# Kernel tuning notes

Hardware: AMD Instinct MI355X
Metric: run time of the kernel (lower is better)

The kernel has to match this reference:

```python
import jax, jax.numpy as jnp
import numpy as np

S, X, G = 2048, 2048, 2
INPUT_SIZE = (3, 32, 32)
F = int(np.prod(INPUT_SIZE))


def setup_inputs() -> dict:
    key = jax.random.key(0)
    k1, k2, k3 = jax.random.split(key, 3)
    samples = jax.random.normal(k1, (S,) + INPUT_SIZE, dtype=jnp.float32)
    x = jax.random.normal(k2, (X,) + INPUT_SIZE, dtype=jnp.float32)
    # per-feature std per gradation, kept in [0.1, 1.0) like ranges_std scaling
    std = jax.random.uniform(k3, (G, F), dtype=jnp.float32, minval=0.1, maxval=1.0)
    return {"samples": samples, "x": x, "std": std}


def reference(samples, x, std):
    # samples: [S, C, H, W], x: [X, C, H, W], std: [G, F]
    G_, F_ = std.shape
    s = samples.reshape(samples.shape[0], F_)  # [S, F]
    xf = x.reshape(x.shape[0], F_)             # [X, F]
    w = 1.0 / (std * std)                       # [G, F] precision
    # per-gradation normalizer: -0.5*F*log(2pi) - sum_f log(std)
    const = -0.5 * F_ * jnp.log(2.0 * jnp.pi) - jnp.sum(jnp.log(std), axis=1)  # [G]
    # sum_f -0.5*((s-x)/std)^2 expanded: -0.5*(s^2 w - 2 s w x + x^2 w)
    A = jnp.einsum('sf,gf->gs', s * s, w)        # [G, S]
    C = jnp.einsum('xf,gf->gx', xf * xf, w)      # [G, X]
    B = jnp.einsum('sf,gf,xf->gsx', s, w, xf)    # [G, S, X] cross term
    logits = -0.5 * (A[:, :, None] - 2.0 * B + C[:, None, :]) + const[:, None, None]
    lp = jax.nn.logsumexp(logits, axis=2)        # over x (mixture components)
    lp = jax.nn.logsumexp(lp, axis=0)            # over gradations
    return lp - jnp.log(jnp.float32(x.shape[0] * G_))
```

## Files before the change

### kernel.cpp

```cpp
#include <hip/hip_runtime.h>
#include <math.h>

#define S_N 2048
#define X_N 2048
#define G_N 2
#define F_N 3072

#define TM 128
#define TN 128
#define BK 64
#define ITERS (F_N / BK)

typedef __bf16 bf16;
typedef __bf16 bf16x4 __attribute__((ext_vector_type(4)));
typedef __bf16 bf16x8 __attribute__((ext_vector_type(8)));
typedef float f32x4 __attribute__((ext_vector_type(4)));
typedef int i32x4 __attribute__((ext_vector_type(4)));

#define LGKM_BARRIER() asm volatile("s_waitcnt lgkmcnt(0)\n\ts_barrier" ::: "memory")

__global__ void k_const(const float* __restrict__ stdv, float* __restrict__ constg,
                        float* __restrict__ rinv) {
  int g = blockIdx.x;
  int t = threadIdx.x;
  float s = 0.f;
  for (int f = t; f < F_N; f += 256) {
    float v = stdv[g * F_N + f];
    rinv[g * F_N + f] = 1.0f / v;
    s += logf(v);
  }
  for (int o = 32; o; o >>= 1) s += __shfl_xor(s, o);
  __shared__ float red[4];
  int w = t >> 6, l = t & 63;
  if (l == 0) red[w] = s;
  __syncthreads();
  if (t == 0) {
    float tot = red[0] + red[1] + red[2] + red[3];
    constg[g] = -0.5f * (float)F_N * 1.8378770664093453f - tot;
  }
}

__global__ void k_prep(const float* __restrict__ samples, const float* __restrict__ xin,
                       const float* __restrict__ rinv,
                       bf16* __restrict__ U, bf16* __restrict__ V,
                       float* __restrict__ A, float* __restrict__ C) {
  int r = blockIdx.x;
  int t = threadIdx.x;
  bool isS = (r < S_N);
  const float* src = isS ? (samples + (size_t)r * F_N) : (xin + (size_t)(r - S_N) * F_N);
  float4 row[3];
#pragma unroll
  for (int j = 0; j < 3; ++j) row[j] = ((const float4*)src)[t + j * 256];

  __shared__ float red[4];
  int w = t >> 6, l = t & 63;

  for (int g = 0; g < G_N; ++g) {
    const float4* sd = (const float4*)(rinv + (size_t)g * F_N);
    bf16* dst = isS ? (U + ((size_t)g * S_N + r) * F_N)
                    : (V + ((size_t)g * X_N + (r - S_N)) * F_N);
    float acc = 0.f;
#pragma unroll
    for (int j = 0; j < 3; ++j) {
      float4 d = sd[t + j * 256];
      float u0 = row[j].x * d.x;
      float u1 = row[j].y * d.y;
      float u2 = row[j].z * d.z;
      float u3 = row[j].w * d.w;
      bf16x4 b;
      b[0] = (bf16)u0; b[1] = (bf16)u1; b[2] = (bf16)u2; b[3] = (bf16)u3;
      float f0 = (float)b[0], f1 = (float)b[1], f2 = (float)b[2], f3 = (float)b[3];
      acc += f0 * f0 + f1 * f1 + f2 * f2 + f3 * f3;
      ((bf16x4*)dst)[t + j * 256] = b;
    }
    for (int o = 32; o; o >>= 1) acc += __shfl_xor(acc, o);
    __syncthreads();
    if (l == 0) red[w] = acc;
    __syncthreads();
    if (t == 0) {
      float tot = red[0] + red[1] + red[2] + red[3];
      if (isS) A[(size_t)g * S_N + r] = tot;
      else     C[(size_t)g * X_N + (r - S_N)] = tot;
    }
  }
}

__global__ __launch_bounds__(256, 2) void k_gemm(const bf16* __restrict__ U, const bf16* __restrict__ V,
                                                 const float* __restrict__ A, const float* __restrict__ C,
                                                 float* __restrict__ logits) {
  __shared__ i32x4 ldsA[2][TM * BK / 8];
  __shared__ i32x4 ldsB[2][TN * BK / 8];

  int t = threadIdx.x;
  int g = blockIdx.z;
  int bm = blockIdx.y * TM;
  int bn = blockIdx.x * TN;

  const bf16* Ub = U + ((size_t)g * S_N + bm) * F_N;
  const bf16* Vb = V + ((size_t)g * X_N + bn) * F_N;

  int wave = t >> 6, lane = t & 63;
  int wm = wave & 1, wn = wave >> 1;
  int r = lane & 15, q = lane >> 4;
  int fr = (r >> 1) & 7;
  int ck0 = q ^ fr;
  int ck1 = (4 | q) ^ fr;

  int row0 = t >> 3;
  int gcc = (t & 7) ^ ((t >> 4) & 7);
  const bf16* gA[4];
  const bf16* gB[4];
#pragma unroll
  for (int j = 0; j < 4; ++j) {
    gA[j] = Ub + (size_t)(row0 + j * 32) * F_N + gcc * 8;
    gB[j] = Vb + (size_t)(row0 + j * 32) * F_N + gcc * 8;
  }

  f32x4 acc[4][4] = {};
  int abase = (wm * 64 + r) * 8;
  int bbase = (wn * 64 + r) * 8;

  i32x4 sA0[4], sB0[4], sA1[4], sB1[4];

#pragma unroll
  for (int j = 0; j < 4; ++j) {
    sA0[j] = *(const i32x4*)(gA[j]);
    sB0[j] = *(const i32x4*)(gB[j]);
  }
#pragma unroll
  for (int j = 0; j < 4; ++j) {
    sA1[j] = *(const i32x4*)(gA[j] + BK);
    sB1[j] = *(const i32x4*)(gB[j] + BK);
  }
#pragma unroll
  for (int j = 0; j < 4; ++j) {
    ldsA[0][t + j * 256] = sA0[j];
    ldsB[0][t + j * 256] = sB0[j];
  }
  LGKM_BARRIER();

  for (int it = 0; it < ITERS; it += 2) {
    {
      int k2 = it + 2;
      int pk = (k2 < ITERS ? k2 : 0) * BK;
#pragma unroll
      for (int j = 0; j < 4; ++j) {
        sA0[j] = *(const i32x4*)(gA[j] + pk);
        sB0[j] = *(const i32x4*)(gB[j] + pk);
      }
#pragma unroll
      for (int ks = 0; ks < 2; ++ks) {
        int ck = ks ? ck1 : ck0;
        bf16x8 af[4], bfr[4];
#pragma unroll
        for (int mi = 0; mi < 4; ++mi)
          af[mi] = __builtin_bit_cast(bf16x8, ldsA[0][abase + mi * 128 + ck]);
#pragma unroll
        for (int ni = 0; ni < 4; ++ni)
          bfr[ni] = __builtin_bit_cast(bf16x8, ldsB[0][bbase + ni * 128 + ck]);
#pragma unroll
        for (int mi = 0; mi < 4; ++mi)
#pragma unroll
          for (int ni = 0; ni < 4; ++ni)
            acc[mi][ni] = __builtin_amdgcn_mfma_f32_16x16x32_bf16(af[mi], bfr[ni], acc[mi][ni], 0, 0, 0);
      }
#pragma unroll
      for (int j = 0; j < 4; ++j) {
        ldsA[1][t + j * 256] = sA1[j];
        ldsB[1][t + j * 256] = sB1[j];
      }
      LGKM_BARRIER();
    }
    {
      int k3 = it + 3;
      int pk = (k3 < ITERS ? k3 : 0) * BK;
#pragma unroll
      for (int j = 0; j < 4; ++j) {
        sA1[j] = *(const i32x4*)(gA[j] + pk);
        sB1[j] = *(const i32x4*)(gB[j] + pk);
      }
#pragma unroll
      for (int ks = 0; ks < 2; ++ks) {
        int ck = ks ? ck1 : ck0;
        bf16x8 af[4], bfr[4];
#pragma unroll
        for (int mi = 0; mi < 4; ++mi)
          af[mi] = __builtin_bit_cast(bf16x8, ldsA[1][abase + mi * 128 + ck]);
#pragma unroll
        for (int ni = 0; ni < 4; ++ni)
          bfr[ni] = __builtin_bit_cast(bf16x8, ldsB[1][bbase + ni * 128 + ck]);
#pragma unroll
        for (int mi = 0; mi < 4; ++mi)
#pragma unroll
          for (int ni = 0; ni < 4; ++ni)
            acc[mi][ni] = __builtin_amdgcn_mfma_f32_16x16x32_bf16(af[mi], bfr[ni], acc[mi][ni], 0, 0, 0);
      }
#pragma unroll
      for (int j = 0; j < 4; ++j) {
        ldsA[0][t + j * 256] = sA0[j];
        ldsB[0][t + j * 256] = sB0[j];
      }
      LGKM_BARRIER();
    }
  }

  const float* Ap = A + (size_t)g * S_N + bm + wm * 64;
  const float* Cp = C + (size_t)g * X_N + bn + wn * 64;
  float cv[4];
#pragma unroll
  for (int ni = 0; ni < 4; ++ni) cv[ni] = Cp[ni * 16 + r];
#pragma unroll
  for (int mi = 0; mi < 4; ++mi) {
#pragma unroll
    for (int i = 0; i < 4; ++i) {
      int rowl = wm * 64 + mi * 16 + q * 4 + i;
      float av = Ap[mi * 16 + q * 4 + i];
      float* orow = logits + ((size_t)g * S_N + bm + rowl) * X_N + bn + wn * 64;
#pragma unroll
      for (int ni = 0; ni < 4; ++ni)
        orow[ni * 16 + r] = acc[mi][ni][i] - 0.5f * (av + cv[ni]);
    }
  }
}

__global__ void k_lse(const float* __restrict__ logits, const float* __restrict__ constg,
                      float* __restrict__ out) {
  int s = blockIdx.x, t = threadIdx.x;
  float c0 = constg[0], c1 = constg[1];
  const float4* p0 = (const float4*)(logits + (size_t)s * X_N);
  const float4* p1 = (const float4*)(logits + ((size_t)S_N + s) * X_N);
  float4 v[4];
  v[0] = p0[t]; v[1] = p0[t + 256];
  v[2] = p1[t]; v[3] = p1[t + 256];
  v[0].x += c0; v[0].y += c0; v[0].z += c0; v[0].w += c0;
  v[1].x += c0; v[1].y += c0; v[1].z += c0; v[1].w += c0;
  v[2].x += c1; v[2].y += c1; v[2].z += c1; v[2].w += c1;
  v[3].x += c1; v[3].y += c1; v[3].z += c1; v[3].w += c1;

  float m = v[0].x;
#pragma unroll
  for (int j = 0; j < 4; ++j) {
    m = fmaxf(m, v[j].x); m = fmaxf(m, v[j].y);
    m = fmaxf(m, v[j].z); m = fmaxf(m, v[j].w);
  }
  for (int o = 32; o; o >>= 1) m = fmaxf(m, __shfl_xor(m, o));
  __shared__ float redm[4];
  __shared__ float reds[4];
  int w = t >> 6, l = t & 63;
  if (l == 0) redm[w] = m;
  __syncthreads();
  m = fmaxf(fmaxf(redm[0], redm[1]), fmaxf(redm[2], redm[3]));

  float sum = 0.f;
#pragma unroll
  for (int j = 0; j < 4; ++j) {
    sum += expf(v[j].x - m) + expf(v[j].y - m) + expf(v[j].z - m) + expf(v[j].w - m);
  }
  for (int o = 32; o; o >>= 1) sum += __shfl_xor(sum, o);
  if (l == 0) reds[w] = sum;
  __syncthreads();
  if (t == 0) {
    float tot = reds[0] + reds[1] + reds[2] + reds[3];
    out[s] = m + logf(tot) - 8.317766166719343f;
  }
}

extern "C" void kernel_launch(void* const* d_in, const int* in_sizes, int n_in,
                              void* d_out, int out_size, void* d_ws, size_t ws_size,
                              hipStream_t stream) {
  const float* samples = (const float*)d_in[0];
  const float* xin     = (const float*)d_in[1];
  const float* stdv    = (const float*)d_in[2];
  float* out = (float*)d_out;

  char* ws = (char*)d_ws;
  size_t off = 0;
  bf16* U = (bf16*)(ws + off);        off += (size_t)G_N * S_N * F_N * 2;
  bf16* V = (bf16*)(ws + off);        off += (size_t)G_N * X_N * F_N * 2;
  float* logits = (float*)(ws + off); off += (size_t)G_N * S_N * X_N * 4;
  float* A = (float*)(ws + off);      off += (size_t)G_N * S_N * 4;
  float* C = (float*)(ws + off);      off += (size_t)G_N * X_N * 4;
  float* constg = (float*)(ws + off); off += 256;
  float* rinv = (float*)(ws + off);   off += (size_t)G_N * F_N * 4;

  k_const<<<dim3(G_N), dim3(256), 0, stream>>>(stdv, constg, rinv);
  k_prep<<<dim3(S_N + X_N), dim3(256), 0, stream>>>(samples, xin, rinv, U, V, A, C);
  k_gemm<<<dim3(X_N / TN, S_N / TM, G_N), dim3(256), 0, stream>>>(U, V, A, C, logits);
  k_lse<<<dim3(S_N), dim3(256), 0, stream>>>(logits, constg, out);
}
```

Baseline: 162.9 us.

## Fuse logsumexp into GEMM epilogue and drop logits buffer and const kernel

The GEMM epilogue now computes per-tile row max and sum-exp using shuffles and LDS, and writes small partial (max, sum) arrays instead of the full G×S×X logits matrix. A new final kernel computes the log-std constants itself and merges the partials across column blocks and gradations. The separate k_const kernel is removed and the reciprocal of std is taken inline with a hardware rcp. This avoids writing and re-reading about 32 MB of logits and removes one launch, at the cost of extra exp work in the GEMM epilogue and a slightly less exact reciprocal.

```diff
diff --git a/kernel.cpp b/kernel.cpp
--- a/kernel.cpp
+++ b/kernel.cpp
@@ -10,6 +10,7 @@
 #define TN 128
 #define BK 64
 #define ITERS (F_N / BK)
+#define NB (X_N / TN)
 
 typedef __bf16 bf16;
 typedef __bf16 bf16x4 __attribute__((ext_vector_type(4)));
@@ -19,29 +20,8 @@
 
 #define LGKM_BARRIER() asm volatile("s_waitcnt lgkmcnt(0)\n\ts_barrier" ::: "memory")
 
-__global__ void k_const(const float* __restrict__ stdv, float* __restrict__ constg,
-                        float* __restrict__ rinv) {
-  int g = blockIdx.x;
-  int t = threadIdx.x;
-  float s = 0.f;
-  for (int f = t; f < F_N; f += 256) {
-    float v = stdv[g * F_N + f];
-    rinv[g * F_N + f] = 1.0f / v;
-    s += logf(v);
-  }
-  for (int o = 32; o; o >>= 1) s += __shfl_xor(s, o);
-  __shared__ float red[4];
-  int w = t >> 6, l = t & 63;
-  if (l == 0) red[w] = s;
-  __syncthreads();
-  if (t == 0) {
-    float tot = red[0] + red[1] + red[2] + red[3];
-    constg[g] = -0.5f * (float)F_N * 1.8378770664093453f - tot;
-  }
-}
-
 __global__ void k_prep(const float* __restrict__ samples, const float* __restrict__ xin,
-                       const float* __restrict__ rinv,
+                       const float* __restrict__ stdv,
                        bf16* __restrict__ U, bf16* __restrict__ V,
                        float* __restrict__ A, float* __restrict__ C) {
   int r = blockIdx.x;
@@ -56,17 +36,17 @@
   int w = t >> 6, l = t & 63;
 
   for (int g = 0; g < G_N; ++g) {
-    const float4* sd = (const float4*)(rinv + (size_t)g * F_N);
+    const float4* sd = (const float4*)(stdv + (size_t)g * F_N);
     bf16* dst = isS ? (U + ((size_t)g * S_N + r) * F_N)
                     : (V + ((size_t)g * X_N + (r - S_N)) * F_N);
     float acc = 0.f;
 #pragma unroll
     for (int j = 0; j < 3; ++j) {
       float4 d = sd[t + j * 256];
-      float u0 = row[j].x * d.x;
-      float u1 = row[j].y * d.y;
-      float u2 = row[j].z * d.z;
-      float u3 = row[j].w * d.w;
+      float u0 = row[j].x * __builtin_amdgcn_rcpf(d.x);
+      float u1 = row[j].y * __builtin_amdgcn_rcpf(d.y);
+      float u2 = row[j].z * __builtin_amdgcn_rcpf(d.z);
+      float u3 = row[j].w * __builtin_amdgcn_rcpf(d.w);
       bf16x4 b;
       b[0] = (bf16)u0; b[1] = (bf16)u1; b[2] = (bf16)u2; b[3] = (bf16)u3;
       float f0 = (float)b[0], f1 = (float)b[1], f2 = (float)b[2], f3 = (float)b[3];
@@ -87,9 +67,11 @@
 
 __global__ __launch_bounds__(256, 2) void k_gemm(const bf16* __restrict__ U, const bf16* __restrict__ V,
                                                  const float* __restrict__ A, const float* __restrict__ C,
-                                                 float* __restrict__ logits) {
+                                                 float* __restrict__ pm, float* __restrict__ ps) {
   __shared__ i32x4 ldsA[2][TM * BK / 8];
   __shared__ i32x4 ldsB[2][TN * BK / 8];
+  __shared__ float lms[2][TM];
+  __shared__ float lss[2][TM];
 
   int t = threadIdx.x;
   int g = blockIdx.z;
@@ -209,60 +191,93 @@
   float cv[4];
 #pragma unroll
   for (int ni = 0; ni < 4; ++ni) cv[ni] = Cp[ni * 16 + r];
+
+  float mloc[4][4], sloc[4][4];
 #pragma unroll
   for (int mi = 0; mi < 4; ++mi) {
 #pragma unroll
     for (int i = 0; i < 4; ++i) {
-      int rowl = wm * 64 + mi * 16 + q * 4 + i;
       float av = Ap[mi * 16 + q * 4 + i];
-      float* orow = logits + ((size_t)g * S_N + bm + rowl) * X_N + bn + wn * 64;
-#pragma unroll
-      for (int ni = 0; ni < 4; ++ni)
-        orow[ni * 16 + r] = acc[mi][ni][i] - 0.5f * (av + cv[ni]);
-    }
+      float l0 = acc[mi][0][i] - 0.5f * (av + cv[0]);
+      float l1 = acc[mi][1][i] - 0.5f * (av + cv[1]);
+      float l2 = acc[mi][2][i] - 0.5f * (av + cv[2]);
+      float l3 = acc[mi][3][i] - 0.5f * (av + cv[3]);
+      float m = fmaxf(fmaxf(l0, l1), fmaxf(l2, l3));
+      m = fmaxf(m, __shfl_xor(m, 1));
+      m = fmaxf(m, __shfl_xor(m, 2));
+      m = fmaxf(m, __shfl_xor(m, 4));
+      m = fmaxf(m, __shfl_xor(m, 8));
+      float s = expf(l0 - m) + expf(l1 - m) + expf(l2 - m) + expf(l3 - m);
+      s += __shfl_xor(s, 1);
+      s += __shfl_xor(s, 2);
+      s += __shfl_xor(s, 4);
+      s += __shfl_xor(s, 8);
+      mloc[mi][i] = m;
+      sloc[mi][i] = s;
+    }
+  }
+  if (r == 0) {
+#pragma unroll
+    for (int mi = 0; mi < 4; ++mi)
+#pragma unroll
+      for (int i = 0; i < 4; ++i) {
+        int rowl = wm * 64 + mi * 16 + q * 4 + i;
+        lms[wn][rowl] = mloc[mi][i];
+        lss[wn][rowl] = sloc[mi][i];
+      }
+  }
+  __syncthreads();
+  if (t < TM) {
+    float m0 = lms[0][t], m1 = lms[1][t];
+    float s0 = lss[0][t], s1 = lss[1][t];
+    float M = fmaxf(m0, m1);
+    float S = s0 * expf(m0 - M) + s1 * expf(m1 - M);
+    size_t idx = ((size_t)g * NB + blockIdx.x) * S_N + bm + t;
+    pm[idx] = M;
+    ps[idx] = S;
   }
 }
 
-__global__ void k_lse(const float* __restrict__ logits, const float* __restrict__ constg,
-                      float* __restrict__ out) {
-  int s = blockIdx.x, t = threadIdx.x;
-  float c0 = constg[0], c1 = constg[1];
-  const float4* p0 = (const float4*)(logits + (size_t)s * X_N);
-  const float4* p1 = (const float4*)(logits + ((size_t)S_N + s) * X_N);
-  float4 v[4];
-  v[0] = p0[t]; v[1] = p0[t + 256];
-  v[2] = p1[t]; v[3] = p1[t + 256];
-  v[0].x += c0; v[0].y += c0; v[0].z += c0; v[0].w += c0;
-  v[1].x += c0; v[1].y += c0; v[1].z += c0; v[1].w += c0;
-  v[2].x += c1; v[2].y += c1; v[2].z += c1; v[2].w += c1;
-  v[3].x += c1; v[3].y += c1; v[3].z += c1; v[3].w += c1;
-
-  float m = v[0].x;
-#pragma unroll
-  for (int j = 0; j < 4; ++j) {
-    m = fmaxf(m, v[j].x); m = fmaxf(m, v[j].y);
-    m = fmaxf(m, v[j].z); m = fmaxf(m, v[j].w);
-  }
-  for (int o = 32; o; o >>= 1) m = fmaxf(m, __shfl_xor(m, o));
-  __shared__ float redm[4];
-  __shared__ float reds[4];
-  int w = t >> 6, l = t & 63;
-  if (l == 0) redm[w] = m;
-  __syncthreads();
-  m = fmaxf(fmaxf(redm[0], redm[1]), fmaxf(redm[2], redm[3]));
-
-  float sum = 0.f;
-#pragma unroll
-  for (int j = 0; j < 4; ++j) {
-    sum += expf(v[j].x - m) + expf(v[j].y - m) + expf(v[j].z - m) + expf(v[j].w - m);
-  }
-  for (int o = 32; o; o >>= 1) sum += __shfl_xor(sum, o);
-  if (l == 0) reds[w] = sum;
-  __syncthreads();
-  if (t == 0) {
-    float tot = reds[0] + reds[1] + reds[2] + reds[3];
-    out[s] = m + logf(tot) - 8.317766166719343f;
-  }
+__global__ void k_final(const float* __restrict__ stdv,
+                        const float* __restrict__ pm, const float* __restrict__ ps,
+                        float* __restrict__ out) {
+  int t = threadIdx.x;
+  int s = blockIdx.x * 256 + t;
+
+  __shared__ float cgs[G_N];
+  __shared__ float red[4];
+  for (int g = 0; g < G_N; ++g) {
+    float a = 0.f;
+    for (int f = t; f < F_N; f += 256) a += logf(stdv[g * F_N + f]);
+    for (int o = 32; o; o >>= 1) a += __shfl_xor(a, o);
+    __syncthreads();
+    if ((t & 63) == 0) red[t >> 6] = a;
+    __syncthreads();
+    if (t == 0) cgs[g] = -0.5f * (float)F_N * 1.8378770664093453f
+                         - (red[0] + red[1] + red[2] + red[3]);
+    __syncthreads();
+  }
+  float cg[G_N];
+#pragma unroll
+  for (int g = 0; g < G_N; ++g) cg[g] = cgs[g];
+
+  float mv[G_N][NB];
+  float M = -INFINITY;
+#pragma unroll
+  for (int g = 0; g < G_N; ++g)
+#pragma unroll
+    for (int cb = 0; cb < NB; ++cb) {
+      float m = pm[((size_t)g * NB + cb) * S_N + s] + cg[g];
+      mv[g][cb] = m;
+      M = fmaxf(M, m);
+    }
+  float T = 0.f;
+#pragma unroll
+  for (int g = 0; g < G_N; ++g)
+#pragma unroll
+    for (int cb = 0; cb < NB; ++cb)
+      T += ps[((size_t)g * NB + cb) * S_N + s] * expf(mv[g][cb] - M);
+  out[s] = M + logf(T) - 8.317766166719343f;
 }
 
 extern "C" void kernel_launch(void* const* d_in, const int* in_sizes, int n_in,
@@ -275,16 +290,14 @@
 
   char* ws = (char*)d_ws;
   size_t off = 0;
-  bf16* U = (bf16*)(ws + off);        off += (size_t)G_N * S_N * F_N * 2;
-  bf16* V = (bf16*)(ws + off);        off += (size_t)G_N * X_N * F_N * 2;
-  float* logits = (float*)(ws + off); off += (size_t)G_N * S_N * X_N * 4;
-  float* A = (float*)(ws + off);      off += (size_t)G_N * S_N * 4;
-  float* C = (float*)(ws + off);      off += (size_t)G_N * X_N * 4;
-  float* constg = (float*)(ws + off); off += 256;
-  float* rinv = (float*)(ws + off);   off += (size_t)G_N * F_N * 4;
-
-  k_const<<<dim3(G_N), dim3(256), 0, stream>>>(stdv, constg, rinv);
-  k_prep<<<dim3(S_N + X_N), dim3(256), 0, stream>>>(samples, xin, rinv, U, V, A, C);
-  k_gemm<<<dim3(X_N / TN, S_N / TM, G_N), dim3(256), 0, stream>>>(U, V, A, C, logits);
-  k_lse<<<dim3(S_N), dim3(256), 0, stream>>>(logits, constg, out);
+  bf16* U = (bf16*)(ws + off);     off += (size_t)G_N * S_N * F_N * 2;
+  bf16* V = (bf16*)(ws + off);     off += (size_t)G_N * X_N * F_N * 2;
+  float* A = (float*)(ws + off);   off += (size_t)G_N * S_N * 4;
+  float* C = (float*)(ws + off);   off += (size_t)G_N * X_N * 4;
+  float* pm = (float*)(ws + off);  off += (size_t)G_N * NB * S_N * 4;
+  float* ps = (float*)(ws + off);  off += (size_t)G_N * NB * S_N * 4;
+
+  k_prep<<<dim3(S_N + X_N), dim3(256), 0, stream>>>(samples, xin, stdv, U, V, A, C);
+  k_gemm<<<dim3(X_N / TN, S_N / TM, G_N), dim3(256), 0, stream>>>(U, V, A, C, pm, ps);
+  k_final<<<dim3(S_N / 256), dim3(256), 0, stream>>>(stdv, pm, ps, out);
 }
```

Measured after the change: 165.3 us. About the same (+1.5%).
